# Kernel optimization log

Hardware: AMD Instinct MI355X
Metric: run time of the kernel (lower is better)

## Reference

```python
import jax, jax.numpy as jnp
import numpy as np

H = 768            # hidden_size
IMG_H = 1024       # image_hidden_size
NH = 12            # num_heads
NKV = 1            # num_kv_heads (MQA)
HD = H // NH       # head_dim = 64
FF = 4 * H         # intermediate_size = 3072
EPS = 1e-5


def layernorm(x, g, b):
    m = jnp.mean(x, axis=-1, keepdims=True)
    v = jnp.mean(jnp.square(x - m), axis=-1, keepdims=True)
    return (x - m) * jax.lax.rsqrt(v + EPS) * g + b


def setup_inputs() -> dict:
    key = jax.random.key(0)
    ks = jax.random.split(key, 12)
    B, NQ, NIMG = 8, 256, 4096
    s = 0.02
    return {
        "hidden_states": jax.random.normal(ks[0], (B, NQ, H), jnp.float32),
        "image_features": jax.random.normal(ks[1], (B, NIMG, IMG_H), jnp.float32),
        # norm_image_pre
        "ln_img_g": jnp.ones((IMG_H,), jnp.float32),
        "ln_img_b": jnp.zeros((IMG_H,), jnp.float32),
        # image_bottleneck (bias=False)
        "W_bottle": jax.random.normal(ks[2], (IMG_H, H), jnp.float32) * s,
        # norm_hidden
        "ln_h_g": jnp.ones((H,), jnp.float32),
        "ln_h_b": jnp.zeros((H,), jnp.float32),
        # to_q
        "Wq": jax.random.normal(ks[3], (H, H), jnp.float32) * s,
        "bq": jnp.zeros((H,), jnp.float32),
        # to_kv: out = num_kv_heads * head_dim * 2
        "Wkv": jax.random.normal(ks[4], (H, 2 * NKV * HD), jnp.float32) * s,
        "bkv": jnp.zeros((2 * NKV * HD,), jnp.float32),
        # to_out
        "Wo": jax.random.normal(ks[5], (H, H), jnp.float32) * s,
        "bo": jnp.zeros((H,), jnp.float32),
        # attn_out_norm
        "ln_ao_g": jnp.ones((H,), jnp.float32),
        "ln_ao_b": jnp.zeros((H,), jnp.float32),
        # gate
        "gate_param": jnp.zeros((), jnp.float32),
        # ffn_norm
        "ln_f_g": jnp.ones((H,), jnp.float32),
        "ln_f_b": jnp.zeros((H,), jnp.float32),
        # ffn
        "W1": jax.random.normal(ks[6], (H, FF), jnp.float32) * s,
        "b1": jnp.zeros((FF,), jnp.float32),
        "W2": jax.random.normal(ks[7], (FF, H), jnp.float32) * s,
        "b2": jnp.zeros((H,), jnp.float32),
    }


def reference(hidden_states, image_features, ln_img_g, ln_img_b, W_bottle,
              ln_h_g, ln_h_b, Wq, bq, Wkv, bkv, Wo, bo, ln_ao_g, ln_ao_b,
              gate_param, ln_f_g, ln_f_b, W1, b1, W2, b2):
    B, NQ, _ = hidden_states.shape
    # image pre-norm + bottleneck
    img = layernorm(image_features, ln_img_g, ln_img_b)
    img = img @ W_bottle                                   # [B, Nimg, H]
    # query path
    q_in = layernorm(hidden_states, ln_h_g, ln_h_b)
    q = (q_in @ Wq + bq).reshape(B, NQ, NH, HD).transpose(0, 2, 1, 3)  # b h i d
    # kv path (MQA: single shared KV head)
    kv = (img @ Wkv + bkv).reshape(B, -1, 2, NKV, HD)
    k = kv[:, :, 0, 0, :]                                  # [B, Nimg, HD]
    v = kv[:, :, 1, 0, :]
    scale = 1.0 / np.sqrt(HD)
    # broadcast KV across heads instead of explicit repeat
    scores = jnp.einsum('bhid,bjd->bhij', q * scale, k)    # [B, NH, NQ, Nimg]
    attn = jax.nn.softmax(scores, axis=-1)                 # dropout is identity (eval)
    out = jnp.einsum('bhij,bjd->bhid', attn, v)
    out = out.transpose(0, 2, 1, 3).reshape(B, NQ, H)
    out = out @ Wo + bo
    out = layernorm(out, ln_ao_g, ln_ao_b)
    gate = jax.nn.sigmoid(gate_param)
    h = hidden_states + gate * out
    ffn_in = layernorm(h, ln_f_g, ln_f_b)
    ffn_out = jax.nn.gelu(ffn_in @ W1 + b1, approximate=False) @ W2 + b2
    return h + ffn_out
```

## Files before the change

### kernel.cpp

```cpp
#include <hip/hip_runtime.h>
#include <cstdint>

typedef unsigned short u16;
typedef __bf16 bf16_t;
typedef bf16_t bf16x8 __attribute__((ext_vector_type(8)));
typedef float f32x4 __attribute__((ext_vector_type(4)));

__device__ __forceinline__ float b2f(u16 v) {
  union { uint32_t u; float f; } c; c.u = ((uint32_t)v) << 16; return c.f;
}
__device__ __forceinline__ u16 f2b(float f) {
  union { float f; uint32_t u; } c; c.f = f;
  uint32_t lsb = (c.u >> 16) & 1u;
  return (u16)((c.u + 0x7fffu + lsb) >> 16);
}
__device__ __forceinline__ uint4 pack8(f32x4 a, f32x4 b) {
  union { uint4 v; u16 s[8]; } r;
  r.s[0] = f2b(a[0]); r.s[1] = f2b(a[1]); r.s[2] = f2b(a[2]); r.s[3] = f2b(a[3]);
  r.s[4] = f2b(b[0]); r.s[5] = f2b(b[1]); r.s[6] = f2b(b[2]); r.s[7] = f2b(b[3]);
  return r.v;
}
__device__ __forceinline__ uint32_t cvt_pk_bf16(float lo, float hi) {
  uint32_t r;
  asm("v_cvt_pk_bf16_f32 %0, %1, %2" : "=v"(r) : "v"(lo), "v"(hi));
  return r;
}
__device__ __forceinline__ void phase_barrier() {
  asm volatile("s_waitcnt lgkmcnt(0)" ::: "memory");
  __builtin_amdgcn_s_barrier();
  asm volatile("" ::: "memory");
}
__device__ __forceinline__ void vm_drain() {
  asm volatile("s_waitcnt vmcnt(0)" ::: "memory");
}
template <int N>
__device__ __forceinline__ void vmwait() {
  asm volatile("s_waitcnt vmcnt(%0)" :: "n"(N) : "memory");
}
__device__ __forceinline__ void gload_lds16(const u16* g, u16* l) {
  __builtin_amdgcn_global_load_lds((const __attribute__((address_space(1))) void*)g,
                                   (__attribute__((address_space(3))) void*)l, 16, 0, 0);
}
__device__ __forceinline__ int xcd_swizzle(int lid, int nwg) {
  int q = nwg >> 3, r = nwg & 7, x = lid & 7, s = lid >> 3;
  return (x < r ? x * (q + 1) : r * (q + 1) + (x - r) * q) + s;
}

__global__ __launch_bounds__(256) void transpose_all(
    const float* __restrict__ Wq, const float* __restrict__ Wo, const float* __restrict__ W1,
    const float* __restrict__ W2, const float* __restrict__ Wkv,
    u16* __restrict__ WTq, u16* __restrict__ WTo, u16* __restrict__ WT1,
    u16* __restrict__ WT2, u16* __restrict__ WkvT) {
  __shared__ __align__(16) u16 tile[32][33];
  int bid = blockIdx.x;
  const float* in; u16* out; int R, C, gx, tb;
  if (bid < 576)       { in = Wq;  out = WTq;  R = 768;  C = 768;  gx = 24; tb = bid; }
  else if (bid < 1152) { in = Wo;  out = WTo;  R = 768;  C = 768;  gx = 24; tb = bid - 576; }
  else if (bid < 3456) { in = W1;  out = WT1;  R = 768;  C = 3072; gx = 96; tb = bid - 1152; }
  else if (bid < 5760) { in = W2;  out = WT2;  R = 3072; C = 768;  gx = 24; tb = bid - 3456; }
  else                 { in = Wkv; out = WkvT; R = 768;  C = 128;  gx = 4;  tb = bid - 5760; }
  int c0 = (tb % gx) * 32, r0 = (tb / gx) * 32;
  int tx = threadIdx.x & 31, ty = threadIdx.x >> 5;
#pragma unroll
  for (int i = 0; i < 4; ++i) {
    int r = r0 + ty + i * 8, c = c0 + tx;
    tile[ty + i * 8][tx] = f2b(in[(size_t)r * C + c]);
  }
  __syncthreads();
#pragma unroll
  for (int i = 0; i < 4; ++i) {
    int oc = c0 + ty + i * 8, orr = r0 + tx;
    out[(size_t)oc * R + orr] = tile[tx][ty + i * 8];
  }
}

__global__ __launch_bounds__(256) void prep_wg2(
    const u16* __restrict__ WTq, const float* __restrict__ gq, const float* __restrict__ bq_,
    u16* __restrict__ WqgT, float* __restrict__ uq, float* __restrict__ wq,
    const u16* __restrict__ WT1, const float* __restrict__ g1, const float* __restrict__ b1_,
    u16* __restrict__ W1gT, float* __restrict__ u1, float* __restrict__ w1) {
  int bid = blockIdx.x;
  const u16* WT; const float* g; const float* b; u16* WgT; float* u; float* w; int n0;
  if (bid < 192) { WT = WTq; g = gq; b = bq_; WgT = WqgT; u = uq; w = wq; n0 = bid * 4; }
  else { WT = WT1; g = g1; b = b1_; WgT = W1gT; u = u1; w = w1; n0 = (bid - 192) * 4; }
  int n = n0 + (threadIdx.x >> 6);
  int lane = threadIdx.x & 63;
  const u16* src = WT + (size_t)n * 768;
  u16* dst = WgT + (size_t)n * 768;
  float su = 0.f, sw = 0.f;
  for (int k = lane; k < 768; k += 64) {
    float wc = b2f(src[k]);
    float wg = g[k] * wc;
    dst[k] = f2b(wg);
    su += wg;
    sw += b[k] * wc;
  }
#pragma unroll
  for (int off = 32; off >= 1; off >>= 1) {
    su += __shfl_xor(su, off, 64);
    sw += __shfl_xor(sw, off, 64);
  }
  if (lane == 0) { u[n] = su; w[n] = sw; }
}

__global__ __launch_bounds__(256) void prep_wg(const u16* __restrict__ WT, const float* __restrict__ g,
                                               const float* __restrict__ b, u16* __restrict__ WgT,
                                               float* __restrict__ ucol, float* __restrict__ wcol,
                                               int K) {
  int n = blockIdx.x * 4 + (threadIdx.x >> 6);
  int lane = threadIdx.x & 63;
  const u16* src = WT + (size_t)n * K;
  u16* dst = WgT + (size_t)n * K;
  float su = 0.f, sw = 0.f;
  for (int k = lane; k < K; k += 64) {
    float wc = b2f(src[k]);
    float wg = g[k] * wc;
    dst[k] = f2b(wg);
    su += wg;
    sw += b[k] * wc;
  }
#pragma unroll
  for (int off = 32; off >= 1; off >>= 1) {
    su += __shfl_xor(su, off, 64);
    sw += __shfl_xor(sw, off, 64);
  }
  if (lane == 0) { ucol[n] = su; wcol[n] = sw; }
}

__global__ __launch_bounds__(256) void rowprep(
    const float* __restrict__ hs, u16* __restrict__ hs16,
    float* __restrict__ rstdq, float* __restrict__ mrstdq,
    const float* __restrict__ img, u16* __restrict__ img16,
    float* __restrict__ rstdi, float* __restrict__ mrstdi) {
  int bid = blockIdx.x, w = threadIdx.x >> 6, lane = threadIdx.x & 63;
  if (bid < 512) {
    int row = bid * 4 + w;
    const float* x = hs + (size_t)row * 768;
    float v[12];
#pragma unroll
    for (int it = 0; it < 3; ++it) {
      f32x4 d = *(const f32x4*)(x + (lane + it * 64) * 4);
      v[it * 4 + 0] = d[0]; v[it * 4 + 1] = d[1]; v[it * 4 + 2] = d[2]; v[it * 4 + 3] = d[3];
    }
    float s = 0.f, s2 = 0.f;
#pragma unroll
    for (int i = 0; i < 12; ++i) { s += v[i]; s2 += v[i] * v[i]; }
#pragma unroll
    for (int off = 32; off >= 1; off >>= 1) {
      s += __shfl_xor(s, off, 64);
      s2 += __shfl_xor(s2, off, 64);
    }
    float inv_n = 1.0f / 768.f;
    float mean = s * inv_n;
    float var = fmaxf(s2 * inv_n - mean * mean, 0.f);
    float rstd = rsqrtf(var + 1e-5f);
    if (lane == 0) { rstdq[row] = rstd; mrstdq[row] = mean * rstd; }
#pragma unroll
    for (int it = 0; it < 3; ++it) {
      int c = (lane + it * 64) * 4;
      uint2 po;
      po.x = (uint32_t)f2b(v[it * 4 + 0]) | ((uint32_t)f2b(v[it * 4 + 1]) << 16);
      po.y = (uint32_t)f2b(v[it * 4 + 2]) | ((uint32_t)f2b(v[it * 4 + 3]) << 16);
      *(uint2*)(hs16 + (size_t)row * 768 + c) = po;
    }
  } else {
    int row = (bid - 512) * 4 + w;
    const float* x = img + (size_t)row * 1024;
    float v[16];
#pragma unroll
    for (int it = 0; it < 4; ++it) {
      f32x4 d = *(const f32x4*)(x + (lane + it * 64) * 4);
      v[it * 4 + 0] = d[0]; v[it * 4 + 1] = d[1]; v[it * 4 + 2] = d[2]; v[it * 4 + 3] = d[3];
    }
    float s = 0.f, s2 = 0.f;
#pragma unroll
    for (int i = 0; i < 16; ++i) { s += v[i]; s2 += v[i] * v[i]; }
#pragma unroll
    for (int off = 32; off >= 1; off >>= 1) {
      s += __shfl_xor(s, off, 64);
      s2 += __shfl_xor(s2, off, 64);
    }
    float inv_n = 1.0f / 1024.f;
    float mean = s * inv_n;
    float var = fmaxf(s2 * inv_n - mean * mean, 0.f);
    float rstd = rsqrtf(var + 1e-5f);
    if (lane == 0) { rstdi[row] = rstd; mrstdi[row] = mean * rstd; }
#pragma unroll
    for (int it = 0; it < 4; ++it) {
      int c = (lane + it * 64) * 4;
      uint2 po;
      po.x = (uint32_t)f2b(v[it * 4 + 0]) | ((uint32_t)f2b(v[it * 4 + 1]) << 16);
      po.y = (uint32_t)f2b(v[it * 4 + 2]) | ((uint32_t)f2b(v[it * 4 + 3]) << 16);
      *(uint2*)(img16 + (size_t)row * 1024 + c) = po;
    }
  }
}

__global__ __launch_bounds__(256) void ln_res(const u16* __restrict__ ao, const float* __restrict__ g,
                                              const float* __restrict__ bta,
                                              const float* __restrict__ hs,
                                              const float* __restrict__ gatep,
                                              float* __restrict__ hf, u16* __restrict__ hb,
                                              float* __restrict__ rstdg, float* __restrict__ mrstdg) {
  int row = blockIdx.x * 4 + (threadIdx.x >> 6);
  int lane = threadIdx.x & 63;
  const u16* xb = ao + (size_t)row * 768;
  float v[12];
#pragma unroll
  for (int it = 0; it < 3; ++it) {
    int c = (lane + it * 64) * 4;
    uint2 d = *(const uint2*)(xb + c);
    v[it * 4 + 0] = b2f(d.x & 0xffff); v[it * 4 + 1] = b2f(d.x >> 16);
    v[it * 4 + 2] = b2f(d.y & 0xffff); v[it * 4 + 3] = b2f(d.y >> 16);
  }
  float s = 0.f, s2 = 0.f;
#pragma unroll
  for (int i = 0; i < 12; ++i) { s += v[i]; s2 += v[i] * v[i]; }
#pragma unroll
  for (int off = 32; off >= 1; off >>= 1) {
    s += __shfl_xor(s, off, 64);
    s2 += __shfl_xor(s2, off, 64);
  }
  float inv_n = 1.0f / 768.f;
  float mean = s * inv_n;
  float var = fmaxf(s2 * inv_n - mean * mean, 0.f);
  float rstd = rsqrtf(var + 1e-5f);
  float gate = 1.f / (1.f + __expf(-gatep[0]));
  float hsum = 0.f, hsum2 = 0.f;
  float o[12];
#pragma unroll
  for (int it = 0; it < 3; ++it) {
    int c = (lane + it * 64) * 4;
    const float* rr = hs + (size_t)row * 768 + c;
#pragma unroll
    for (int i = 0; i < 4; ++i) {
      float hv = rr[i] + gate * ((v[it * 4 + i] - mean) * rstd * g[c + i] + bta[c + i]);
      o[it * 4 + i] = hv;
      hsum += hv; hsum2 += hv * hv;
    }
    *(f32x4*)(hf + (size_t)row * 768 + c) = (f32x4){o[it * 4 + 0], o[it * 4 + 1], o[it * 4 + 2], o[it * 4 + 3]};
    uint2 po;
    po.x = (uint32_t)f2b(o[it * 4 + 0]) | ((uint32_t)f2b(o[it * 4 + 1]) << 16);
    po.y = (uint32_t)f2b(o[it * 4 + 2]) | ((uint32_t)f2b(o[it * 4 + 3]) << 16);
    *(uint2*)(hb + (size_t)row * 768 + c) = po;
  }
#pragma unroll
  for (int off = 32; off >= 1; off >>= 1) {
    hsum += __shfl_xor(hsum, off, 64);
    hsum2 += __shfl_xor(hsum2, off, 64);
  }
  float hm = hsum * inv_n;
  float hvar = fmaxf(hsum2 * inv_n - hm * hm, 0.f);
  float hrstd = rsqrtf(hvar + 1e-5f);
  if (lane == 0) { rstdg[row] = hrstd; mrstdg[row] = hm * hrstd; }
}

template <int BM, int SPLITK, int AMODE, int BMODE, int EPI, bool OUTF32, bool VTOUT>
__device__ __forceinline__ void gemm_body(const void* __restrict__ Av, const void* __restrict__ Bv,
                                          const float* __restrict__ bias,
                                          const float* __restrict__ rstdg,
                                          const float* __restrict__ mrstdg,
                                          const float* __restrict__ ucol,
                                          const float* __restrict__ wcol,
                                          void* __restrict__ Cv, u16* __restrict__ VTout,
                                          int M, int N, int K) {
  constexpr int MT = BM / 32;
  constexpr int AL = BM / 64;
  constexpr bool PURE = (AMODE == 0 && BMODE == 0);
  constexpr int NBUF = PURE ? 4 : 2;
  constexpr int LPT = AL + 2;
  __shared__ __align__(16) u16 aT[NBUF][BM * 32];
  __shared__ __align__(16) u16 bT[NBUF][128 * 32];

  int gx = gridDim.x, gy = gridDim.y;
  int nwg = gx * gy * (int)gridDim.z;
  int lid = ((int)blockIdx.z * gy + (int)blockIdx.y) * gx + (int)blockIdx.x;
  int wid = xcd_swizzle(lid, nwg);
  int bz = wid / (gx * gy);
  int rem = wid - bz * (gx * gy);
  int bx = rem / gy;
  int by = rem - bx * gy;

  int t = threadIdx.x, lane = t & 63, wave = t >> 6;
  int quad = lane >> 4, lcol = lane & 15;
  int wm = (wave >> 1) * (16 * MT), wn = (wave & 1) * 64;
  const u16* Ab = (const u16*)Av;
  const u16* Bb = (const u16*)Bv;
  const float* Bf = (const float*)Bv;
  const int kchunk = (SPLITK > 1) ? K / SPLITK : K;
  const int kstart = (SPLITK > 1) ? bz * kchunk : 0;
  int rr = t >> 1, rc = t & 1;
  f32x4 acc[MT][4];
#pragma unroll
  for (int i = 0; i < MT; ++i)
#pragma unroll
    for (int j = 0; j < 4; ++j) acc[i][j] = (f32x4){0.f, 0.f, 0.f, 0.f};

  f32x4 braw[4];

  auto dmaA = [&](int buf, int k0) {
#pragma unroll
    for (int s2 = 0; s2 < AL; ++s2) {
      int row = (wave * AL + s2) * 16 + (lane >> 2);
      int ch = (lane & 3) ^ (row & 3);
      gload_lds16(Ab + (size_t)(bx * BM + row) * K + kstart + k0 + ch * 8,
                  &aT[buf][(wave * AL + s2) * 512]);
    }
  };
  auto dmaB = [&](int buf, int k0) {
#pragma unroll
    for (int s2 = 0; s2 < 2; ++s2) {
      int row = (wave * 2 + s2) * 16 + (lane >> 2);
      int ch = (lane & 3) ^ (row & 3);
      gload_lds16(Bb + (size_t)(by * 128 + row) * K + kstart + k0 + ch * 8,
                  &bT[buf][(wave * 2 + s2) * 512]);
    }
  };
  auto regloadB = [&](int k0) {
    const f32x4* p = (const f32x4*)&Bf[(size_t)(by * 128 + rr) * K + kstart + k0 + rc * 16];
#pragma unroll
    for (int i = 0; i < 4; ++i) braw[i] = p[i];
  };
  auto regstoreB = [&](int buf) {
    uint4 c0 = pack8(braw[0], braw[1]), c1 = pack8(braw[2], braw[3]);
    *(uint4*)&bT[buf][rr * 32 + (((rc * 2 + 0) ^ (rr & 3)) << 3)] = c0;
    *(uint4*)&bT[buf][rr * 32 + (((rc * 2 + 1) ^ (rr & 3)) << 3)] = c1;
  };
  auto compute = [&](int buf) {
    bf16x8 af[MT], bfr[4];
#pragma unroll
    for (int mt = 0; mt < MT; ++mt) {
      int r = wm + mt * 16 + lcol;
      af[mt] = *(const bf16x8*)&aT[buf][r * 32 + (((quad ^ (r & 3))) << 3)];
    }
#pragma unroll
    for (int nt = 0; nt < 4; ++nt) {
      int r = wn + nt * 16 + lcol;
      bfr[nt] = *(const bf16x8*)&bT[buf][r * 32 + (((quad ^ (r & 3))) << 3)];
    }
#pragma unroll
    for (int mt = 0; mt < MT; ++mt)
#pragma unroll
      for (int nt = 0; nt < 4; ++nt)
        acc[mt][nt] = __builtin_amdgcn_mfma_f32_16x16x32_bf16(af[mt], bfr[nt], acc[mt][nt], 0, 0, 0);
  };

  const int nk = kchunk >> 5;
  if (PURE) {
    dmaA(0, 0); dmaB(0, 0);
    if (nk > 1) { dmaA(1, 1 << 5); dmaB(1, 1 << 5); }
    if (nk > 2) { dmaA(2, 2 << 5); dmaB(2, 2 << 5); }
    for (int kt = 0; kt < nk; ++kt) {
      int left = nk - 1 - kt;
      if (left >= 2) vmwait<2 * LPT>();
      else if (left == 1) vmwait<LPT>();
      else vmwait<0>();
      phase_barrier();
      if (kt + 3 < nk) { dmaA((kt + 3) & 3, (kt + 3) << 5); dmaB((kt + 3) & 3, (kt + 3) << 5); }
      compute(kt & 3);
    }
  } else {
    dmaA(0, 0);
    regloadB(0);
    regstoreB(0);
    vm_drain();
    phase_barrier();
    int cur = 0;
    for (int kt = 0; kt < nk; ++kt) {
      bool more = kt + 1 < nk;
      if (more) { dmaA(cur ^ 1, (kt + 1) << 5); regloadB((kt + 1) << 5); }
      compute(cur);
      if (more) regstoreB(cur ^ 1);
      vm_drain();
      phase_barrier();
      cur ^= 1;
    }
  }

  if (VTOUT) {
    __syncthreads();
    u16* vtile = &aT[0][0];
    u16* kb = (u16*)Cv;
#pragma unroll
    for (int mt = 0; mt < MT; ++mt) {
#pragma unroll
      for (int nt = 0; nt < 4; ++nt) {
#pragma unroll
        for (int r = 0; r < 4; ++r) {
          int lrow = wm + mt * 16 + quad * 4 + r;
          int row = bx * BM + lrow;
          int col = wn + nt * 16 + lcol;
          float v = rstdg[row] * acc[mt][nt][r] - mrstdg[row] * ucol[col] + wcol[col] + bias[col];
          u16 hv = f2b(v);
          if (wn == 0) kb[(size_t)row * 64 + col] = hv;
          else vtile[(col - 64) * 136 + lrow] = hv;
        }
      }
    }
    __syncthreads();
    int dd = t >> 2, js = (t & 3) * 32;
    int bg = bx >> 5, j0g = (bx & 31) * 128;
    u16* dst = VTout + ((size_t)bg * 64 + dd) * 4096 + j0g + js;
#pragma unroll
    for (int i = 0; i < 4; ++i)
      *(uint4*)(dst + i * 8) = *(const uint4*)&vtile[dd * 136 + js + i * 8];
    return;
  }

  u16* Cb = (u16*)Cv;
  float* Cf = (float*)Cv;
  if (SPLITK > 1) Cf += (size_t)bz * (size_t)M * (size_t)N;
#pragma unroll
  for (int mt = 0; mt < MT; ++mt) {
#pragma unroll
    for (int nt = 0; nt < 4; ++nt) {
#pragma unroll
      for (int r = 0; r < 4; ++r) {
        int lrow = wm + mt * 16 + quad * 4 + r;
        int row = bx * BM + lrow;
        int col = by * 128 + wn + nt * 16 + lcol;
        float v = acc[mt][nt][r];
        if (EPI == 1) v += bias[col];
        if (EPI == 3 || EPI == 5)
          v = rstdg[row] * v - mrstdg[row] * ucol[col] + wcol[col] + bias[col];
        if (EPI == 5) v = 0.5f * v * (1.f + erff(v * 0.70710678118f));
        size_t idx = (size_t)row * N + col;
        if (OUTF32) Cf[idx] = v; else Cb[idx] = f2b(v);
      }
    }
  }
}

#define GEMM_ARGS const void* Av, const void* Bv, const float* bias, const float* rstdg, \
                  const float* mrstdg, const float* ucol, const float* wcol, void* Cv,   \
                  u16* VTout, int M, int N, int K
__global__ __launch_bounds__(256) void gemm_wc(GEMM_ARGS) {
  gemm_body<128, 1, 0, 1, 0, false, false>(Av, Bv, bias, rstdg, mrstdg, ucol, wcol, Cv, VTout, M, N, K);
}
__global__ __launch_bounds__(256) void gemm_kv(GEMM_ARGS) {
  gemm_body<128, 1, 0, 0, 3, false, true>(Av, Bv, bias, rstdg, mrstdg, ucol, wcol, Cv, VTout, M, N, K);
}
__global__ __launch_bounds__(256) void gemm_q(GEMM_ARGS) {
  gemm_body<64, 1, 0, 0, 3, false, false>(Av, Bv, bias, rstdg, mrstdg, ucol, wcol, Cv, VTout, M, N, K);
}
__global__ __launch_bounds__(256) void gemm_o(GEMM_ARGS) {
  gemm_body<64, 1, 0, 0, 1, false, false>(Av, Bv, bias, rstdg, mrstdg, ucol, wcol, Cv, VTout, M, N, K);
}
__global__ __launch_bounds__(256) void gemm_w1(GEMM_ARGS) {
  gemm_body<128, 1, 0, 0, 5, false, false>(Av, Bv, bias, rstdg, mrstdg, ucol, wcol, Cv, VTout, M, N, K);
}
__global__ __launch_bounds__(256) void gemm_w2(GEMM_ARGS) {
  gemm_body<128, 2, 0, 0, 0, true, false>(Av, Bv, bias, rstdg, mrstdg, ucol, wcol, Cv, VTout, M, N, K);
}

__global__ __launch_bounds__(256) void w2_merge(const float* __restrict__ part,
                                                const float* __restrict__ hf,
                                                const float* __restrict__ b2,
                                                float* __restrict__ out) {
  int idx = blockIdx.x * 256 + threadIdx.x;
  f32x4 p0 = ((const f32x4*)part)[idx];
  f32x4 p1 = ((const f32x4*)part)[idx + 393216];
  f32x4 h = ((const f32x4*)hf)[idx];
  f32x4 bb = ((const f32x4*)b2)[idx % 192];
  f32x4 o;
#pragma unroll
  for (int i = 0; i < 4; ++i) o[i] = p0[i] + p1[i] + h[i] + bb[i];
  ((f32x4*)out)[idx] = o;
}

__global__ __launch_bounds__(256) void attn_kernel(const u16* __restrict__ qbuf,
                                                   const u16* __restrict__ kb,
                                                   const u16* __restrict__ VT,
                                                   float* __restrict__ Opart,
                                                   float* __restrict__ lpart) {
  __shared__ __align__(16) u16 k_lds[2][64 * 72];
  __shared__ __align__(16) u16 vt_lds[2][64 * 72];
  __shared__ __align__(16) u16 p_lds[4 * 16 * 72];
  int lid = ((int)blockIdx.z * 6 + (int)blockIdx.y) * 4 + (int)blockIdx.x;
  int wid = (lid & 7) * 96 + (lid >> 3);
  int bi = wid & 3;
  int hp = (wid >> 2) % 6;
  int z = wid / 24;
  int b = z >> 2, s = z & 3;
  int t = threadIdx.x;
  int wave = t >> 6, lane = t & 63, quad = lane >> 4, lcol = lane & 15;
  int i0 = bi * 64 + wave * 16;
  bf16x8 qf[2][2];
#pragma unroll
  for (int h2 = 0; h2 < 2; ++h2) {
    const u16* qrow = qbuf + ((size_t)(b * 256 + i0 + lcol) * 768 + (hp * 2 + h2) * 64 + quad * 8);
    qf[h2][0] = *(const bf16x8*)qrow;
    qf[h2][1] = *(const bf16x8*)(qrow + 32);
  }
  float l_r[2][4] = {{0.f, 0.f, 0.f, 0.f}, {0.f, 0.f, 0.f, 0.f}};
  f32x4 oacc[2][4];
#pragma unroll
  for (int h2 = 0; h2 < 2; ++h2)
#pragma unroll
    for (int nt = 0; nt < 4; ++nt) oacc[h2][nt] = (f32x4){0.f, 0.f, 0.f, 0.f};
  int sr = t >> 2, sc = (t & 3) * 16;
  const u16* kbase = kb + (size_t)b * 4096 * 64;
  const u16* vtbase = VT + (size_t)b * 64 * 4096;
  u16* pw = &p_lds[wave * 16 * 72];

  uint4 kr0, kr1, vr0, vr1;
  auto stage_load = [&](int jt) {
    int j0 = s * 1024 + jt * 64;
    const u16* krow = kbase + (size_t)(j0 + sr) * 64 + sc;
    kr0 = *(const uint4*)(krow);
    kr1 = *(const uint4*)(krow + 8);
    const u16* vrow = vtbase + (size_t)sr * 4096 + j0 + sc;
    vr0 = *(const uint4*)(vrow);
    vr1 = *(const uint4*)(vrow + 8);
  };
  auto stage_store = [&](int buf) {
    *(uint4*)&k_lds[buf][sr * 72 + sc] = kr0;
    *(uint4*)&k_lds[buf][sr * 72 + sc + 8] = kr1;
    *(uint4*)&vt_lds[buf][sr * 72 + sc] = vr0;
    *(uint4*)&vt_lds[buf][sr * 72 + sc + 8] = vr1;
  };

  stage_load(0);
  stage_store(0);
  phase_barrier();
  int cur = 0;
  for (int jt = 0; jt < 16; ++jt) {
    bool more = jt + 1 < 16;
    if (more) stage_load(jt + 1);

#pragma unroll
    for (int h2 = 0; h2 < 2; ++h2) {
      f32x4 sc4[4];
#pragma unroll
      for (int nt = 0; nt < 4; ++nt) sc4[nt] = (f32x4){0.f, 0.f, 0.f, 0.f};
      __builtin_amdgcn_s_setprio(1);
#pragma unroll
      for (int nt = 0; nt < 4; ++nt) {
        bf16x8 kb0 = *(const bf16x8*)&k_lds[cur][(nt * 16 + lcol) * 72 + quad * 8];
        bf16x8 kb1 = *(const bf16x8*)&k_lds[cur][(nt * 16 + lcol) * 72 + 32 + quad * 8];
        sc4[nt] = __builtin_amdgcn_mfma_f32_16x16x32_bf16(qf[h2][0], kb0, sc4[nt], 0, 0, 0);
        sc4[nt] = __builtin_amdgcn_mfma_f32_16x16x32_bf16(qf[h2][1], kb1, sc4[nt], 0, 0, 0);
      }
      __builtin_amdgcn_s_setprio(0);
#pragma unroll
      for (int r = 0; r < 4; ++r) {
        float rsum = 0.f;
#pragma unroll
        for (int nt = 0; nt < 4; ++nt) {
          float p = __expf(sc4[nt][r] * 0.125f);
          sc4[nt][r] = p;
          rsum += p;
        }
        rsum += __shfl_xor(rsum, 1, 64);
        rsum += __shfl_xor(rsum, 2, 64);
        rsum += __shfl_xor(rsum, 4, 64);
        rsum += __shfl_xor(rsum, 8, 64);
        l_r[h2][r] += rsum;
        uint32_t pk01 = cvt_pk_bf16(sc4[0][r], sc4[1][r]);
        uint32_t pk23 = cvt_pk_bf16(sc4[2][r], sc4[3][r]);
        int prow = (quad * 4 + r) * 72 + lcol;
        pw[prow] = (u16)(pk01 & 0xffff);
        pw[prow + 16] = (u16)(pk01 >> 16);
        pw[prow + 32] = (u16)(pk23 & 0xffff);
        pw[prow + 48] = (u16)(pk23 >> 16);
      }
      __builtin_amdgcn_s_setprio(1);
#pragma unroll
      for (int ks = 0; ks < 2; ++ks) {
        bf16x8 pa = *(const bf16x8*)&pw[lcol * 72 + ks * 32 + quad * 8];
#pragma unroll
        for (int nt = 0; nt < 4; ++nt) {
          bf16x8 vb = *(const bf16x8*)&vt_lds[cur][(nt * 16 + lcol) * 72 + ks * 32 + quad * 8];
          oacc[h2][nt] = __builtin_amdgcn_mfma_f32_16x16x32_bf16(pa, vb, oacc[h2][nt], 0, 0, 0);
        }
      }
      __builtin_amdgcn_s_setprio(0);
    }
    if (more) stage_store(cur ^ 1);
    phase_barrier();
    cur ^= 1;
  }
#pragma unroll
  for (int h2 = 0; h2 < 2; ++h2) {
    size_t base = ((size_t)z * 12 + hp * 2 + h2) * 256;
#pragma unroll
    for (int r = 0; r < 4; ++r) {
      int row = bi * 64 + wave * 16 + quad * 4 + r;
#pragma unroll
      for (int nt = 0; nt < 4; ++nt)
        Opart[(base + row) * 64 + nt * 16 + lcol] = oacc[h2][nt][r];
      if (lcol == 0) lpart[base + row] = l_r[h2][r];
    }
  }
}

__global__ __launch_bounds__(256) void attn_merge(const float* __restrict__ Opart,
                                                  const float* __restrict__ lpart,
                                                  u16* __restrict__ attn_o) {
  int row = blockIdx.x;
  int col = blockIdx.y * 256 + threadIdx.x;
  int b = row >> 8, i = row & 255, h = col >> 6, d = col & 63;
  float o = 0.f, l = 0.f;
#pragma unroll
  for (int s = 0; s < 4; ++s) {
    size_t ii = (((size_t)(b * 4 + s) * 12 + h) * 256 + i);
    o += Opart[ii * 64 + d];
    l += lpart[ii];
  }
  attn_o[(size_t)row * 768 + col] = f2b(o / l);
}

extern "C" void kernel_launch(void* const* d_in, const int* in_sizes, int n_in, void* d_out,
                              int out_size, void* d_ws, size_t ws_size, hipStream_t stream) {
  (void)in_sizes; (void)n_in; (void)out_size; (void)ws_size;
  const float* hs = (const float*)d_in[0];
  const float* imgf = (const float*)d_in[1];
  const float* ln_img_g = (const float*)d_in[2];
  const float* ln_img_b = (const float*)d_in[3];
  const float* W_bottle = (const float*)d_in[4];
  const float* ln_h_g = (const float*)d_in[5];
  const float* ln_h_b = (const float*)d_in[6];
  const float* Wq = (const float*)d_in[7];
  const float* bq = (const float*)d_in[8];
  const float* Wkv = (const float*)d_in[9];
  const float* bkv = (const float*)d_in[10];
  const float* Wo = (const float*)d_in[11];
  const float* bo = (const float*)d_in[12];
  const float* ln_ao_g = (const float*)d_in[13];
  const float* ln_ao_b = (const float*)d_in[14];
  const float* gatep = (const float*)d_in[15];
  const float* ln_f_g = (const float*)d_in[16];
  const float* ln_f_b = (const float*)d_in[17];
  const float* W1 = (const float*)d_in[18];
  const float* b1 = (const float*)d_in[19];
  const float* W2 = (const float*)d_in[20];
  const float* b2 = (const float*)d_in[21];

  char* sc = (char*)d_ws;
  auto alloc = [&](size_t bytes) {
    char* p = sc;
    sc += (bytes + 63) & ~(size_t)63;
    return p;
  };
  u16* WTq = (u16*)alloc(768 * 768 * 2);
  u16* WTo = (u16*)alloc(768 * 768 * 2);
  u16* WT1 = (u16*)alloc(3072 * 768 * 2);
  u16* WT2 = (u16*)alloc(768 * 3072 * 2);
  u16* WkvT = (u16*)alloc(128 * 768 * 2);
  u16* WcT = (u16*)alloc(128 * 1024 * 2);
  u16* WgT = (u16*)alloc(128 * 1024 * 2);
  u16* WqgT = (u16*)alloc(768 * 768 * 2);
  u16* W1gT = (u16*)alloc(3072 * 768 * 2);
  float* ucol = (float*)alloc(128 * 4);
  float* wcol = (float*)alloc(128 * 4);
  float* uq = (float*)alloc(768 * 4);
  float* wq = (float*)alloc(768 * 4);
  float* u1 = (float*)alloc(3072 * 4);
  float* w1c = (float*)alloc(3072 * 4);
  float* rstdq = (float*)alloc(2048 * 4);
  float* mrstdq = (float*)alloc(2048 * 4);
  float* rstdh = (float*)alloc(2048 * 4);
  float* mrstdh = (float*)alloc(2048 * 4);
  float* rstdi = (float*)alloc(32768 * 4);
  float* mrstdi = (float*)alloc(32768 * 4);
  u16* hs16 = (u16*)alloc(2048 * 768 * 2);
  u16* img16 = (u16*)alloc((size_t)32768 * 1024 * 2);
  u16* kb = (u16*)alloc((size_t)32768 * 64 * 2);
  u16* VT = (u16*)alloc((size_t)8 * 64 * 4096 * 2);
  u16* qb = (u16*)alloc(2048 * 768 * 2);
  u16* attn_o = (u16*)alloc(2048 * 768 * 2);
  u16* ao = (u16*)alloc(2048 * 768 * 2);
  u16* hbuf = (u16*)alloc(2048 * 768 * 2);
  float* hf32 = (float*)alloc(2048 * 768 * 4);
  u16* actb = (u16*)alloc((size_t)2048 * 3072 * 2);
  float* Opart = (float*)alloc((size_t)32 * 12 * 256 * 64 * 4);
  float* lpart = (float*)alloc((size_t)32 * 12 * 256 * 4);

  transpose_all<<<5856, 256, 0, stream>>>(Wq, Wo, W1, W2, Wkv, WTq, WTo, WT1, WT2, WkvT);
  prep_wg2<<<960, 256, 0, stream>>>(WTq, ln_h_g, ln_h_b, WqgT, uq, wq,
                                    WT1, ln_f_g, ln_f_b, W1gT, u1, w1c);
  gemm_wc<<<dim3(1, 8), 256, 0, stream>>>(WkvT, W_bottle, nullptr, nullptr, nullptr, nullptr,
                                          nullptr, WcT, nullptr, 128, 1024, 768);
  prep_wg<<<32, 256, 0, stream>>>(WcT, ln_img_g, ln_img_b, WgT, ucol, wcol, 1024);
  rowprep<<<8704, 256, 0, stream>>>(hs, hs16, rstdq, mrstdq, imgf, img16, rstdi, mrstdi);
  gemm_kv<<<dim3(256, 1), 256, 0, stream>>>(img16, WgT, bkv, rstdi, mrstdi, ucol, wcol,
                                            kb, VT, 32768, 128, 1024);
  gemm_q<<<dim3(32, 6), 256, 0, stream>>>(hs16, WqgT, bq, rstdq, mrstdq, uq, wq,
                                          qb, nullptr, 2048, 768, 768);
  attn_kernel<<<dim3(4, 6, 32), 256, 0, stream>>>(qb, kb, VT, Opart, lpart);
  attn_merge<<<dim3(2048, 3), 256, 0, stream>>>(Opart, lpart, attn_o);
  gemm_o<<<dim3(32, 6), 256, 0, stream>>>(attn_o, WTo, bo, nullptr, nullptr, nullptr, nullptr,
                                          ao, nullptr, 2048, 768, 768);
  ln_res<<<512, 256, 0, stream>>>(ao, ln_ao_g, ln_ao_b, hs, gatep, hf32, hbuf, rstdh, mrstdh);
  gemm_w1<<<dim3(16, 24), 256, 0, stream>>>(hbuf, W1gT, b1, rstdh, mrstdh, u1, w1c,
                                            actb, nullptr, 2048, 3072, 768);
  gemm_w2<<<dim3(16, 6, 2), 256, 0, stream>>>(actb, WT2, nullptr, nullptr, nullptr, nullptr, nullptr,
                                              Opart, nullptr, 2048, 768, 3072);
  w2_merge<<<1536, 256, 0, stream>>>(Opart, hf32, b2, (float*)d_out);
}
```

Baseline: 532.9 us.

## Fuse prep kernels, merge KV and Q GEMMs, fold attention merge into out-projection

The weight transpose and row-normalisation prep kernels become one launch, and the KV and Q projection GEMMs share a single grid through virtual block indexing. The attention split-K merge (summing partial outputs and dividing by the row sum) now happens inside the out-projection GEMM's A-tile loader, which removes the separate merge kernel and its bf16 intermediate buffer. The attention kernel now handles one head per block instead of two, doubling its grid in y. The aim is fewer launches and less global round-tripping, at the cost of a heavier register-path A load in gemm_o and some imbalance between the heterogeneous blocks in the fused launches.

```diff
diff --git a/kernel.cpp b/kernel.cpp
--- a/kernel.cpp
+++ b/kernel.cpp
@@ -46,45 +46,112 @@
   return (x < r ? x * (q + 1) : r * (q + 1) + (x - r) * q) + s;
 }
 
-__global__ __launch_bounds__(256) void transpose_all(
+__global__ __launch_bounds__(256) void prep_main(
     const float* __restrict__ Wq, const float* __restrict__ Wo, const float* __restrict__ W1,
     const float* __restrict__ W2, const float* __restrict__ Wkv,
     u16* __restrict__ WTq, u16* __restrict__ WTo, u16* __restrict__ WT1,
-    u16* __restrict__ WT2, u16* __restrict__ WkvT) {
+    u16* __restrict__ WT2, u16* __restrict__ WkvT,
+    const float* __restrict__ hs, u16* __restrict__ hs16,
+    float* __restrict__ rstdq, float* __restrict__ mrstdq,
+    const float* __restrict__ img, u16* __restrict__ img16,
+    float* __restrict__ rstdi, float* __restrict__ mrstdi) {
   __shared__ __align__(16) u16 tile[32][33];
   int bid = blockIdx.x;
-  const float* in; u16* out; int R, C, gx, tb;
-  if (bid < 576)       { in = Wq;  out = WTq;  R = 768;  C = 768;  gx = 24; tb = bid; }
-  else if (bid < 1152) { in = Wo;  out = WTo;  R = 768;  C = 768;  gx = 24; tb = bid - 576; }
-  else if (bid < 3456) { in = W1;  out = WT1;  R = 768;  C = 3072; gx = 96; tb = bid - 1152; }
-  else if (bid < 5760) { in = W2;  out = WT2;  R = 3072; C = 768;  gx = 24; tb = bid - 3456; }
-  else                 { in = Wkv; out = WkvT; R = 768;  C = 128;  gx = 4;  tb = bid - 5760; }
-  int c0 = (tb % gx) * 32, r0 = (tb / gx) * 32;
-  int tx = threadIdx.x & 31, ty = threadIdx.x >> 5;
-#pragma unroll
-  for (int i = 0; i < 4; ++i) {
-    int r = r0 + ty + i * 8, c = c0 + tx;
-    tile[ty + i * 8][tx] = f2b(in[(size_t)r * C + c]);
-  }
-  __syncthreads();
-#pragma unroll
-  for (int i = 0; i < 4; ++i) {
-    int oc = c0 + ty + i * 8, orr = r0 + tx;
-    out[(size_t)oc * R + orr] = tile[tx][ty + i * 8];
-  }
-}
-
-__global__ __launch_bounds__(256) void prep_wg2(
+  int lane = threadIdx.x & 63, w = threadIdx.x >> 6;
+  if (bid < 5856) {
+    const float* in; u16* out; int R, C, gx, tb;
+    if (bid < 576)       { in = Wq;  out = WTq;  R = 768;  C = 768;  gx = 24; tb = bid; }
+    else if (bid < 1152) { in = Wo;  out = WTo;  R = 768;  C = 768;  gx = 24; tb = bid - 576; }
+    else if (bid < 3456) { in = W1;  out = WT1;  R = 768;  C = 3072; gx = 96; tb = bid - 1152; }
+    else if (bid < 5760) { in = W2;  out = WT2;  R = 3072; C = 768;  gx = 24; tb = bid - 3456; }
+    else                 { in = Wkv; out = WkvT; R = 768;  C = 128;  gx = 4;  tb = bid - 5760; }
+    int c0 = (tb % gx) * 32, r0 = (tb / gx) * 32;
+    int tx = threadIdx.x & 31, ty = threadIdx.x >> 5;
+#pragma unroll
+    for (int i = 0; i < 4; ++i) {
+      int r = r0 + ty + i * 8, c = c0 + tx;
+      tile[ty + i * 8][tx] = f2b(in[(size_t)r * C + c]);
+    }
+    __syncthreads();
+#pragma unroll
+    for (int i = 0; i < 4; ++i) {
+      int oc = c0 + ty + i * 8, orr = r0 + tx;
+      out[(size_t)oc * R + orr] = tile[tx][ty + i * 8];
+    }
+  } else if (bid < 6368) {
+    int row = (bid - 5856) * 4 + w;
+    const float* x = hs + (size_t)row * 768;
+    float v[12];
+#pragma unroll
+    for (int it = 0; it < 3; ++it) {
+      f32x4 d = *(const f32x4*)(x + (lane + it * 64) * 4);
+      v[it * 4 + 0] = d[0]; v[it * 4 + 1] = d[1]; v[it * 4 + 2] = d[2]; v[it * 4 + 3] = d[3];
+    }
+    float s = 0.f, s2 = 0.f;
+#pragma unroll
+    for (int i = 0; i < 12; ++i) { s += v[i]; s2 += v[i] * v[i]; }
+#pragma unroll
+    for (int off = 32; off >= 1; off >>= 1) {
+      s += __shfl_xor(s, off, 64);
+      s2 += __shfl_xor(s2, off, 64);
+    }
+    float inv_n = 1.0f / 768.f;
+    float mean = s * inv_n;
+    float var = fmaxf(s2 * inv_n - mean * mean, 0.f);
+    float rstd = rsqrtf(var + 1e-5f);
+    if (lane == 0) { rstdq[row] = rstd; mrstdq[row] = mean * rstd; }
+#pragma unroll
+    for (int it = 0; it < 3; ++it) {
+      int c = (lane + it * 64) * 4;
+      uint2 po;
+      po.x = (uint32_t)f2b(v[it * 4 + 0]) | ((uint32_t)f2b(v[it * 4 + 1]) << 16);
+      po.y = (uint32_t)f2b(v[it * 4 + 2]) | ((uint32_t)f2b(v[it * 4 + 3]) << 16);
+      *(uint2*)(hs16 + (size_t)row * 768 + c) = po;
+    }
+  } else {
+    int row = (bid - 6368) * 4 + w;
+    const float* x = img + (size_t)row * 1024;
+    float v[16];
+#pragma unroll
+    for (int it = 0; it < 4; ++it) {
+      f32x4 d = *(const f32x4*)(x + (lane + it * 64) * 4);
+      v[it * 4 + 0] = d[0]; v[it * 4 + 1] = d[1]; v[it * 4 + 2] = d[2]; v[it * 4 + 3] = d[3];
+    }
+    float s = 0.f, s2 = 0.f;
+#pragma unroll
+    for (int i = 0; i < 16; ++i) { s += v[i]; s2 += v[i] * v[i]; }
+#pragma unroll
+    for (int off = 32; off >= 1; off >>= 1) {
+      s += __shfl_xor(s, off, 64);
+      s2 += __shfl_xor(s2, off, 64);
+    }
+    float inv_n = 1.0f / 1024.f;
+    float mean = s * inv_n;
+    float var = fmaxf(s2 * inv_n - mean * mean, 0.f);
+    float rstd = rsqrtf(var + 1e-5f);
+    if (lane == 0) { rstdi[row] = rstd; mrstdi[row] = mean * rstd; }
+#pragma unroll
+    for (int it = 0; it < 4; ++it) {
+      int c = (lane + it * 64) * 4;
+      uint2 po;
+      po.x = (uint32_t)f2b(v[it * 4 + 0]) | ((uint32_t)f2b(v[it * 4 + 1]) << 16);
+      po.y = (uint32_t)f2b(v[it * 4 + 2]) | ((uint32_t)f2b(v[it * 4 + 3]) << 16);
+      *(uint2*)(img16 + (size_t)row * 1024 + c) = po;
+    }
+  }
+}
+
+__global__ __launch_bounds__(256) void prep_fold(
     const u16* __restrict__ WTq, const float* __restrict__ gq, const float* __restrict__ bq_,
-    u16* __restrict__ WqgT, float* __restrict__ uq, float* __restrict__ wq,
+    u16* __restrict__ WqgT, float* __restrict__ uq, float* __restrict__ wqv,
     const u16* __restrict__ WT1, const float* __restrict__ g1, const float* __restrict__ b1_,
-    u16* __restrict__ W1gT, float* __restrict__ u1, float* __restrict__ w1) {
-  int bid = blockIdx.x;
-  const u16* WT; const float* g; const float* b; u16* WgT; float* u; float* w; int n0;
-  if (bid < 192) { WT = WTq; g = gq; b = bq_; WgT = WqgT; u = uq; w = wq; n0 = bid * 4; }
-  else { WT = WT1; g = g1; b = b1_; WgT = W1gT; u = u1; w = w1; n0 = (bid - 192) * 4; }
-  int n = n0 + (threadIdx.x >> 6);
-  int lane = threadIdx.x & 63;
+    u16* __restrict__ W1gT, float* __restrict__ u1, float* __restrict__ w1v) {
+  int pid = blockIdx.x;
+  int lane = threadIdx.x & 63, w = threadIdx.x >> 6;
+  const u16* WT; const float* g; const float* b; u16* WgT; float* u; float* wv; int n0;
+  if (pid < 192) { WT = WTq; g = gq; b = bq_; WgT = WqgT; u = uq; wv = wqv; n0 = pid * 4; }
+  else { WT = WT1; g = g1; b = b1_; WgT = W1gT; u = u1; wv = w1v; n0 = (pid - 192) * 4; }
+  int n = n0 + w;
   const u16* src = WT + (size_t)n * 768;
   u16* dst = WgT + (size_t)n * 768;
   float su = 0.f, sw = 0.f;
@@ -100,7 +167,7 @@
     su += __shfl_xor(su, off, 64);
     sw += __shfl_xor(sw, off, 64);
   }
-  if (lane == 0) { u[n] = su; w[n] = sw; }
+  if (lane == 0) { u[n] = su; wv[n] = sw; }
 }
 
 __global__ __launch_bounds__(256) void prep_wg(const u16* __restrict__ WT, const float* __restrict__ g,
@@ -127,75 +194,6 @@
   if (lane == 0) { ucol[n] = su; wcol[n] = sw; }
 }
 
-__global__ __launch_bounds__(256) void rowprep(
-    const float* __restrict__ hs, u16* __restrict__ hs16,
-    float* __restrict__ rstdq, float* __restrict__ mrstdq,
-    const float* __restrict__ img, u16* __restrict__ img16,
-    float* __restrict__ rstdi, float* __restrict__ mrstdi) {
-  int bid = blockIdx.x, w = threadIdx.x >> 6, lane = threadIdx.x & 63;
-  if (bid < 512) {
-    int row = bid * 4 + w;
-    const float* x = hs + (size_t)row * 768;
-    float v[12];
-#pragma unroll
-    for (int it = 0; it < 3; ++it) {
-      f32x4 d = *(const f32x4*)(x + (lane + it * 64) * 4);
-      v[it * 4 + 0] = d[0]; v[it * 4 + 1] = d[1]; v[it * 4 + 2] = d[2]; v[it * 4 + 3] = d[3];
-    }
-    float s = 0.f, s2 = 0.f;
-#pragma unroll
-    for (int i = 0; i < 12; ++i) { s += v[i]; s2 += v[i] * v[i]; }
-#pragma unroll
-    for (int off = 32; off >= 1; off >>= 1) {
-      s += __shfl_xor(s, off, 64);
-      s2 += __shfl_xor(s2, off, 64);
-    }
-    float inv_n = 1.0f / 768.f;
-    float mean = s * inv_n;
-    float var = fmaxf(s2 * inv_n - mean * mean, 0.f);
-    float rstd = rsqrtf(var + 1e-5f);
-    if (lane == 0) { rstdq[row] = rstd; mrstdq[row] = mean * rstd; }
-#pragma unroll
-    for (int it = 0; it < 3; ++it) {
-      int c = (lane + it * 64) * 4;
-      uint2 po;
-      po.x = (uint32_t)f2b(v[it * 4 + 0]) | ((uint32_t)f2b(v[it * 4 + 1]) << 16);
-      po.y = (uint32_t)f2b(v[it * 4 + 2]) | ((uint32_t)f2b(v[it * 4 + 3]) << 16);
-      *(uint2*)(hs16 + (size_t)row * 768 + c) = po;
-    }
-  } else {
-    int row = (bid - 512) * 4 + w;
-    const float* x = img + (size_t)row * 1024;
-    float v[16];
-#pragma unroll
-    for (int it = 0; it < 4; ++it) {
-      f32x4 d = *(const f32x4*)(x + (lane + it * 64) * 4);
-      v[it * 4 + 0] = d[0]; v[it * 4 + 1] = d[1]; v[it * 4 + 2] = d[2]; v[it * 4 + 3] = d[3];
-    }
-    float s = 0.f, s2 = 0.f;
-#pragma unroll
-    for (int i = 0; i < 16; ++i) { s += v[i]; s2 += v[i] * v[i]; }
-#pragma unroll
-    for (int off = 32; off >= 1; off >>= 1) {
-      s += __shfl_xor(s, off, 64);
-      s2 += __shfl_xor(s2, off, 64);
-    }
-    float inv_n = 1.0f / 1024.f;
-    float mean = s * inv_n;
-    float var = fmaxf(s2 * inv_n - mean * mean, 0.f);
-    float rstd = rsqrtf(var + 1e-5f);
-    if (lane == 0) { rstdi[row] = rstd; mrstdi[row] = mean * rstd; }
-#pragma unroll
-    for (int it = 0; it < 4; ++it) {
-      int c = (lane + it * 64) * 4;
-      uint2 po;
-      po.x = (uint32_t)f2b(v[it * 4 + 0]) | ((uint32_t)f2b(v[it * 4 + 1]) << 16);
-      po.y = (uint32_t)f2b(v[it * 4 + 2]) | ((uint32_t)f2b(v[it * 4 + 3]) << 16);
-      *(uint2*)(img16 + (size_t)row * 1024 + c) = po;
-    }
-  }
-}
-
 __global__ __launch_bounds__(256) void ln_res(const u16* __restrict__ ao, const float* __restrict__ g,
                                               const float* __restrict__ bta,
                                               const float* __restrict__ hs,
@@ -256,35 +254,36 @@
 }
 
 template <int BM, int SPLITK, int AMODE, int BMODE, int EPI, bool OUTF32, bool VTOUT>
-__device__ __forceinline__ void gemm_body(const void* __restrict__ Av, const void* __restrict__ Bv,
+__device__ __forceinline__ void gemm_body(u16* __restrict__ aTb, u16* __restrict__ bTb,
+                                          const void* __restrict__ Av, const void* __restrict__ Bv,
                                           const float* __restrict__ bias,
                                           const float* __restrict__ rstdg,
                                           const float* __restrict__ mrstdg,
                                           const float* __restrict__ ucol,
                                           const float* __restrict__ wcol,
+                                          const float* __restrict__ auxl,
                                           void* __restrict__ Cv, u16* __restrict__ VTout,
-                                          int M, int N, int K) {
+                                          int M, int N, int K,
+                                          int vgx, int vgy, int vgz, int vlid) {
   constexpr int MT = BM / 32;
   constexpr int AL = BM / 64;
   constexpr bool PURE = (AMODE == 0 && BMODE == 0);
-  constexpr int NBUF = PURE ? 4 : 2;
   constexpr int LPT = AL + 2;
-  __shared__ __align__(16) u16 aT[NBUF][BM * 32];
-  __shared__ __align__(16) u16 bT[NBUF][128 * 32];
-
-  int gx = gridDim.x, gy = gridDim.y;
-  int nwg = gx * gy * (int)gridDim.z;
-  int lid = ((int)blockIdx.z * gy + (int)blockIdx.y) * gx + (int)blockIdx.x;
-  int wid = xcd_swizzle(lid, nwg);
-  int bz = wid / (gx * gy);
-  int rem = wid - bz * (gx * gy);
-  int bx = rem / gy;
-  int by = rem - bx * gy;
+  constexpr int ASZ = BM * 32;
+  constexpr int BSZ = 128 * 32;
+
+  int nwg = vgx * vgy * vgz;
+  int wid = xcd_swizzle(vlid, nwg);
+  int bz = wid / (vgx * vgy);
+  int rem = wid - bz * (vgx * vgy);
+  int bx = rem / vgy;
+  int by = rem - bx * vgy;
 
   int t = threadIdx.x, lane = t & 63, wave = t >> 6;
   int quad = lane >> 4, lcol = lane & 15;
   int wm = (wave >> 1) * (16 * MT), wn = (wave & 1) * 64;
   const u16* Ab = (const u16*)Av;
+  const float* Af = (const float*)Av;
   const u16* Bb = (const u16*)Bv;
   const float* Bf = (const float*)Bv;
   const int kchunk = (SPLITK > 1) ? K / SPLITK : K;
@@ -297,6 +296,7 @@
     for (int j = 0; j < 4; ++j) acc[i][j] = (f32x4){0.f, 0.f, 0.f, 0.f};
 
   f32x4 braw[4];
+  f32x4 am0, am1;
 
   auto dmaA = [&](int buf, int k0) {
 #pragma unroll
@@ -304,7 +304,7 @@
       int row = (wave * AL + s2) * 16 + (lane >> 2);
       int ch = (lane & 3) ^ (row & 3);
       gload_lds16(Ab + (size_t)(bx * BM + row) * K + kstart + k0 + ch * 8,
-                  &aT[buf][(wave * AL + s2) * 512]);
+                  aTb + buf * ASZ + (wave * AL + s2) * 512);
     }
   };
   auto dmaB = [&](int buf, int k0) {
@@ -313,8 +313,34 @@
       int row = (wave * 2 + s2) * 16 + (lane >> 2);
       int ch = (lane & 3) ^ (row & 3);
       gload_lds16(Bb + (size_t)(by * 128 + row) * K + kstart + k0 + ch * 8,
-                  &bT[buf][(wave * 2 + s2) * 512]);
-    }
+                  bTb + buf * BSZ + (wave * 2 + s2) * 512);
+    }
+  };
+  auto loadAmerge = [&](int k0) {
+    int c0 = kstart + k0 + (t & 3) * 8;
+    int hh = c0 >> 6, dd = c0 & 63;
+    int row = bx * 64 + (t >> 2);
+    int bb = row >> 8, ii = row & 255;
+    am0 = (f32x4){0.f, 0.f, 0.f, 0.f};
+    am1 = (f32x4){0.f, 0.f, 0.f, 0.f};
+    float lsum = 0.f;
+#pragma unroll
+    for (int s = 0; s < 4; ++s) {
+      size_t base = ((size_t)((bb * 4 + s) * 12 + hh)) * 256 + ii;
+      const f32x4* p = (const f32x4*)(Af + base * 64 + dd);
+      f32x4 p0 = p[0], p1 = p[1];
+#pragma unroll
+      for (int j = 0; j < 4; ++j) { am0[j] += p0[j]; am1[j] += p1[j]; }
+      lsum += auxl[base];
+    }
+    float rl = 1.f / lsum;
+#pragma unroll
+    for (int j = 0; j < 4; ++j) { am0[j] *= rl; am1[j] *= rl; }
+  };
+  auto storeAmerge = [&](int buf) {
+    uint4 c = pack8(am0, am1);
+    int ar = t >> 2, ch = t & 3;
+    *(uint4*)(aTb + buf * ASZ + ar * 32 + ((ch ^ (ar & 3)) << 3)) = c;
   };
   auto regloadB = [&](int k0) {
     const f32x4* p = (const f32x4*)&Bf[(size_t)(by * 128 + rr) * K + kstart + k0 + rc * 16];
@@ -323,20 +349,20 @@
   };
   auto regstoreB = [&](int buf) {
     uint4 c0 = pack8(braw[0], braw[1]), c1 = pack8(braw[2], braw[3]);
-    *(uint4*)&bT[buf][rr * 32 + (((rc * 2 + 0) ^ (rr & 3)) << 3)] = c0;
-    *(uint4*)&bT[buf][rr * 32 + (((rc * 2 + 1) ^ (rr & 3)) << 3)] = c1;
+    *(uint4*)(bTb + buf * BSZ + rr * 32 + (((rc * 2 + 0) ^ (rr & 3)) << 3)) = c0;
+    *(uint4*)(bTb + buf * BSZ + rr * 32 + (((rc * 2 + 1) ^ (rr & 3)) << 3)) = c1;
   };
   auto compute = [&](int buf) {
     bf16x8 af[MT], bfr[4];
 #pragma unroll
     for (int mt = 0; mt < MT; ++mt) {
       int r = wm + mt * 16 + lcol;
-      af[mt] = *(const bf16x8*)&aT[buf][r * 32 + (((quad ^ (r & 3))) << 3)];
+      af[mt] = *(const bf16x8*)(aTb + buf * ASZ + r * 32 + (((quad ^ (r & 3))) << 3));
     }
 #pragma unroll
     for (int nt = 0; nt < 4; ++nt) {
       int r = wn + nt * 16 + lcol;
-      bfr[nt] = *(const bf16x8*)&bT[buf][r * 32 + (((quad ^ (r & 3))) << 3)];
+      bfr[nt] = *(const bf16x8*)(bTb + buf * BSZ + r * 32 + (((quad ^ (r & 3))) << 3));
     }
 #pragma unroll
     for (int mt = 0; mt < MT; ++mt)
@@ -360,17 +386,24 @@
       compute(kt & 3);
     }
   } else {
-    dmaA(0, 0);
-    regloadB(0);
-    regstoreB(0);
+    if (AMODE == 2) loadAmerge(0); else dmaA(0, 0);
+    if (BMODE == 1) regloadB(0); else dmaB(0, 0);
+    if (AMODE == 2) storeAmerge(0);
+    if (BMODE == 1) regstoreB(0);
     vm_drain();
     phase_barrier();
     int cur = 0;
     for (int kt = 0; kt < nk; ++kt) {
       bool more = kt + 1 < nk;
-      if (more) { dmaA(cur ^ 1, (kt + 1) << 5); regloadB((kt + 1) << 5); }
+      if (more) {
+        if (AMODE == 2) loadAmerge((kt + 1) << 5); else dmaA(cur ^ 1, (kt + 1) << 5);
+        if (BMODE == 1) regloadB((kt + 1) << 5); else dmaB(cur ^ 1, (kt + 1) << 5);
+      }
       compute(cur);
-      if (more) regstoreB(cur ^ 1);
+      if (more) {
+        if (AMODE == 2) storeAmerge(cur ^ 1);
+        if (BMODE == 1) regstoreB(cur ^ 1);
+      }
       vm_drain();
       phase_barrier();
       cur ^= 1;
@@ -379,7 +412,7 @@
 
   if (VTOUT) {
     __syncthreads();
-    u16* vtile = &aT[0][0];
+    u16* vtile = aTb;
     u16* kb = (u16*)Cv;
 #pragma unroll
     for (int mt = 0; mt < MT; ++mt) {
@@ -431,26 +464,53 @@
   }
 }
 
-#define GEMM_ARGS const void* Av, const void* Bv, const float* bias, const float* rstdg, \
-                  const float* mrstdg, const float* ucol, const float* wcol, void* Cv,   \
-                  u16* VTout, int M, int N, int K
-__global__ __launch_bounds__(256) void gemm_wc(GEMM_ARGS) {
-  gemm_body<128, 1, 0, 1, 0, false, false>(Av, Bv, bias, rstdg, mrstdg, ucol, wcol, Cv, VTout, M, N, K);
-}
-__global__ __launch_bounds__(256) void gemm_kv(GEMM_ARGS) {
-  gemm_body<128, 1, 0, 0, 3, false, true>(Av, Bv, bias, rstdg, mrstdg, ucol, wcol, Cv, VTout, M, N, K);
-}
-__global__ __launch_bounds__(256) void gemm_q(GEMM_ARGS) {
-  gemm_body<64, 1, 0, 0, 3, false, false>(Av, Bv, bias, rstdg, mrstdg, ucol, wcol, Cv, VTout, M, N, K);
-}
-__global__ __launch_bounds__(256) void gemm_o(GEMM_ARGS) {
-  gemm_body<64, 1, 0, 0, 1, false, false>(Av, Bv, bias, rstdg, mrstdg, ucol, wcol, Cv, VTout, M, N, K);
-}
-__global__ __launch_bounds__(256) void gemm_w1(GEMM_ARGS) {
-  gemm_body<128, 1, 0, 0, 5, false, false>(Av, Bv, bias, rstdg, mrstdg, ucol, wcol, Cv, VTout, M, N, K);
-}
-__global__ __launch_bounds__(256) void gemm_w2(GEMM_ARGS) {
-  gemm_body<128, 2, 0, 0, 0, true, false>(Av, Bv, bias, rstdg, mrstdg, ucol, wcol, Cv, VTout, M, N, K);
+__global__ __launch_bounds__(256) void gemm_wc(const void* Av, const void* Bv, void* Cv) {
+  __shared__ __align__(16) u16 lds[16384];
+  int vlid = ((int)blockIdx.y) * 1 + (int)blockIdx.x;
+  gemm_body<128, 1, 0, 1, 0, false, false>(lds, lds + 8192, Av, Bv, nullptr, nullptr, nullptr,
+                                           nullptr, nullptr, nullptr, Cv, nullptr,
+                                           128, 1024, 768, 1, 8, 1, vlid);
+}
+__global__ __launch_bounds__(256) void gemm_kvq(
+    const void* Akv, const void* Bkv, const float* biaskv, const float* rstdi,
+    const float* mrstdi, const float* ui, const float* wi, void* Ckv, u16* VTout,
+    const void* Aq, const void* Bq, const float* biasq, const float* rstdq,
+    const float* mrstdq, const float* uq, const float* wqv, void* Cq) {
+  __shared__ __align__(16) u16 lds[32768];
+  int bid = blockIdx.x;
+  if (bid < 256) {
+    gemm_body<128, 1, 0, 0, 3, false, true>(lds, lds + 16384, Akv, Bkv, biaskv, rstdi, mrstdi,
+                                            ui, wi, nullptr, Ckv, VTout,
+                                            32768, 128, 1024, 256, 1, 1, bid);
+  } else {
+    gemm_body<64, 1, 0, 0, 3, false, false>(lds, lds + 8192, Aq, Bq, biasq, rstdq, mrstdq,
+                                            uq, wqv, nullptr, Cq, nullptr,
+                                            2048, 768, 768, 32, 6, 1, bid - 256);
+  }
+}
+__global__ __launch_bounds__(256) void gemm_o(const void* Av, const void* Bv, const float* bias,
+                                              const float* lpart, void* Cv) {
+  __shared__ __align__(16) u16 lds[12288];
+  int vlid = ((int)blockIdx.y) * 32 + (int)blockIdx.x;
+  gemm_body<64, 1, 2, 0, 1, false, false>(lds, lds + 4096, Av, Bv, bias, nullptr, nullptr,
+                                          nullptr, nullptr, lpart, Cv, nullptr,
+                                          2048, 768, 768, 32, 6, 1, vlid);
+}
+__global__ __launch_bounds__(256) void gemm_w1(const void* Av, const void* Bv, const float* bias,
+                                               const float* rstdg, const float* mrstdg,
+                                               const float* ucol, const float* wcol, void* Cv) {
+  __shared__ __align__(16) u16 lds[32768];
+  int vlid = ((int)blockIdx.y) * 16 + (int)blockIdx.x;
+  gemm_body<128, 1, 0, 0, 5, false, false>(lds, lds + 16384, Av, Bv, bias, rstdg, mrstdg,
+                                           ucol, wcol, nullptr, Cv, nullptr,
+                                           2048, 3072, 768, 16, 24, 1, vlid);
+}
+__global__ __launch_bounds__(256) void gemm_w2(const void* Av, const void* Bv, void* Cv) {
+  __shared__ __align__(16) u16 lds[32768];
+  int vlid = (((int)blockIdx.z) * 6 + (int)blockIdx.y) * 16 + (int)blockIdx.x;
+  gemm_body<128, 2, 0, 0, 0, true, false>(lds, lds + 16384, Av, Bv, nullptr, nullptr, nullptr,
+                                          nullptr, nullptr, nullptr, Cv, nullptr,
+                                          2048, 768, 3072, 16, 6, 2, vlid);
 }
 
 __global__ __launch_bounds__(256) void w2_merge(const float* __restrict__ part,
@@ -476,28 +536,22 @@
   __shared__ __align__(16) u16 k_lds[2][64 * 72];
   __shared__ __align__(16) u16 vt_lds[2][64 * 72];
   __shared__ __align__(16) u16 p_lds[4 * 16 * 72];
-  int lid = ((int)blockIdx.z * 6 + (int)blockIdx.y) * 4 + (int)blockIdx.x;
-  int wid = (lid & 7) * 96 + (lid >> 3);
+  int lid = ((int)blockIdx.z * 12 + (int)blockIdx.y) * 4 + (int)blockIdx.x;
+  int wid = (lid & 7) * 192 + (lid >> 3);
   int bi = wid & 3;
-  int hp = (wid >> 2) % 6;
-  int z = wid / 24;
+  int h = (wid >> 2) % 12;
+  int z = wid / 48;
   int b = z >> 2, s = z & 3;
   int t = threadIdx.x;
   int wave = t >> 6, lane = t & 63, quad = lane >> 4, lcol = lane & 15;
   int i0 = bi * 64 + wave * 16;
-  bf16x8 qf[2][2];
-#pragma unroll
-  for (int h2 = 0; h2 < 2; ++h2) {
-    const u16* qrow = qbuf + ((size_t)(b * 256 + i0 + lcol) * 768 + (hp * 2 + h2) * 64 + quad * 8);
-    qf[h2][0] = *(const bf16x8*)qrow;
-    qf[h2][1] = *(const bf16x8*)(qrow + 32);
-  }
-  float l_r[2][4] = {{0.f, 0.f, 0.f, 0.f}, {0.f, 0.f, 0.f, 0.f}};
-  f32x4 oacc[2][4];
-#pragma unroll
-  for (int h2 = 0; h2 < 2; ++h2)
-#pragma unroll
-    for (int nt = 0; nt < 4; ++nt) oacc[h2][nt] = (f32x4){0.f, 0.f, 0.f, 0.f};
+  const u16* qrow = qbuf + ((size_t)(b * 256 + i0 + lcol) * 768 + h * 64 + quad * 8);
+  bf16x8 qf0 = *(const bf16x8*)qrow;
+  bf16x8 qf1 = *(const bf16x8*)(qrow + 32);
+  float l_r[4] = {0.f, 0.f, 0.f, 0.f};
+  f32x4 oacc[4];
+#pragma unroll
+  for (int nt = 0; nt < 4; ++nt) oacc[nt] = (f32x4){0.f, 0.f, 0.f, 0.f};
   int sr = t >> 2, sc = (t & 3) * 16;
   const u16* kbase = kb + (size_t)b * 4096 * 64;
   const u16* vtbase = VT + (size_t)b * 64 * 4096;
@@ -528,86 +582,64 @@
     bool more = jt + 1 < 16;
     if (more) stage_load(jt + 1);
 
-#pragma unroll
-    for (int h2 = 0; h2 < 2; ++h2) {
-      f32x4 sc4[4];
-#pragma unroll
-      for (int nt = 0; nt < 4; ++nt) sc4[nt] = (f32x4){0.f, 0.f, 0.f, 0.f};
-      __builtin_amdgcn_s_setprio(1);
+    f32x4 sc4[4];
+#pragma unroll
+    for (int nt = 0; nt < 4; ++nt) sc4[nt] = (f32x4){0.f, 0.f, 0.f, 0.f};
+    __builtin_amdgcn_s_setprio(1);
+#pragma unroll
+    for (int nt = 0; nt < 4; ++nt) {
+      bf16x8 kb0 = *(const bf16x8*)&k_lds[cur][(nt * 16 + lcol) * 72 + quad * 8];
+      bf16x8 kb1 = *(const bf16x8*)&k_lds[cur][(nt * 16 + lcol) * 72 + 32 + quad * 8];
+      sc4[nt] = __builtin_amdgcn_mfma_f32_16x16x32_bf16(qf0, kb0, sc4[nt], 0, 0, 0);
+      sc4[nt] = __builtin_amdgcn_mfma_f32_16x16x32_bf16(qf1, kb1, sc4[nt], 0, 0, 0);
+    }
+    __builtin_amdgcn_s_setprio(0);
+#pragma unroll
+    for (int r = 0; r < 4; ++r) {
+      float rsum = 0.f;
 #pragma unroll
       for (int nt = 0; nt < 4; ++nt) {
-        bf16x8 kb0 = *(const bf16x8*)&k_lds[cur][(nt * 16 + lcol) * 72 + quad * 8];
-        bf16x8 kb1 = *(const bf16x8*)&k_lds[cur][(nt * 16 + lcol) * 72 + 32 + quad * 8];
-        sc4[nt] = __builtin_amdgcn_mfma_f32_16x16x32_bf16(qf[h2][0], kb0, sc4[nt], 0, 0, 0);
-        sc4[nt] = __builtin_amdgcn_mfma_f32_16x16x32_bf16(qf[h2][1], kb1, sc4[nt], 0, 0, 0);
+        float p = __expf(sc4[nt][r] * 0.125f);
+        sc4[nt][r] = p;
+        rsum += p;
       }
-      __builtin_amdgcn_s_setprio(0);
-#pragma unroll
-      for (int r = 0; r < 4; ++r) {
-        float rsum = 0.f;
-#pragma unroll
-        for (int nt = 0; nt < 4; ++nt) {
-          float p = __expf(sc4[nt][r] * 0.125f);
-          sc4[nt][r] = p;
-          rsum += p;
-        }
-        rsum += __shfl_xor(rsum, 1, 64);
-        rsum += __shfl_xor(rsum, 2, 64);
-        rsum += __shfl_xor(rsum, 4, 64);
-        rsum += __shfl_xor(rsum, 8, 64);
-        l_r[h2][r] += rsum;
-        uint32_t pk01 = cvt_pk_bf16(sc4[0][r], sc4[1][r]);
-        uint32_t pk23 = cvt_pk_bf16(sc4[2][r], sc4[3][r]);
-        int prow = (quad * 4 + r) * 72 + lcol;
-        pw[prow] = (u16)(pk01 & 0xffff);
-        pw[prow + 16] = (u16)(pk01 >> 16);
-        pw[prow + 32] = (u16)(pk23 & 0xffff);
-        pw[prow + 48] = (u16)(pk23 >> 16);
+      rsum += __shfl_xor(rsum, 1, 64);
+      rsum += __shfl_xor(rsum, 2, 64);
+      rsum += __shfl_xor(rsum, 4, 64);
+      rsum += __shfl_xor(rsum, 8, 64);
+      l_r[r] += rsum;
+      uint32_t pk01 = cvt_pk_bf16(sc4[0][r], sc4[1][r]);
+      uint32_t pk23 = cvt_pk_bf16(sc4[2][r], sc4[3][r]);
+      int prow = (quad * 4 + r) * 72 + lcol;
+      pw[prow] = (u16)(pk01 & 0xffff);
+      pw[prow + 16] = (u16)(pk01 >> 16);
+      pw[prow + 32] = (u16)(pk23 & 0xffff);
+      pw[prow + 48] = (u16)(pk23 >> 16);
+    }
+    __builtin_amdgcn_s_setprio(1);
+#pragma unroll
+    for (int ks = 0; ks < 2; ++ks) {
+      bf16x8 pa = *(const bf16x8*)&pw[lcol * 72 + ks * 32 + quad * 8];
+#pragma unroll
+      for (int nt = 0; nt < 4; ++nt) {
+        bf16x8 vb = *(const bf16x8*)&vt_lds[cur][(nt * 16 + lcol) * 72 + ks * 32 + quad * 8];
+        oacc[nt] = __builtin_amdgcn_mfma_f32_16x16x32_bf16(pa, vb, oacc[nt], 0, 0, 0);
       }
-      __builtin_amdgcn_s_setprio(1);
-#pragma unroll
-      for (int ks = 0; ks < 2; ++ks) {
-        bf16x8 pa = *(const bf16x8*)&pw[lcol * 72 + ks * 32 + quad * 8];
-#pragma unroll
-        for (int nt = 0; nt < 4; ++nt) {
-          bf16x8 vb = *(const bf16x8*)&vt_lds[cur][(nt * 16 + lcol) * 72 + ks * 32 + quad * 8];
-          oacc[h2][nt] = __builtin_amdgcn_mfma_f32_16x16x32_bf16(pa, vb, oacc[h2][nt], 0, 0, 0);
-        }
-      }
-      __builtin_amdgcn_s_setprio(0);
-    }
+    }
+    __builtin_amdgcn_s_setprio(0);
     if (more) stage_store(cur ^ 1);
     phase_barrier();
     cur ^= 1;
   }
-#pragma unroll
-  for (int h2 = 0; h2 < 2; ++h2) {
-    size_t base = ((size_t)z * 12 + hp * 2 + h2) * 256;
-#pragma unroll
-    for (int r = 0; r < 4; ++r) {
-      int row = bi * 64 + wave * 16 + quad * 4 + r;
-#pragma unroll
-      for (int nt = 0; nt < 4; ++nt)
-        Opart[(base + row) * 64 + nt * 16 + lcol] = oacc[h2][nt][r];
-      if (lcol == 0) lpart[base + row] = l_r[h2][r];
-    }
-  }
-}
-
-__global__ __launch_bounds__(256) void attn_merge(const float* __restrict__ Opart,
-                                                  const float* __restrict__ lpart,
-                                                  u16* __restrict__ attn_o) {
-  int row = blockIdx.x;
-  int col = blockIdx.y * 256 + threadIdx.x;
-  int b = row >> 8, i = row & 255, h = col >> 6, d = col & 63;
-  float o = 0.f, l = 0.f;
-#pragma unroll
-  for (int s = 0; s < 4; ++s) {
-    size_t ii = (((size_t)(b * 4 + s) * 12 + h) * 256 + i);
-    o += Opart[ii * 64 + d];
-    l += lpart[ii];
-  }
-  attn_o[(size_t)row * 768 + col] = f2b(o / l);
+  size_t base = ((size_t)z * 12 + h) * 256;
+#pragma unroll
+  for (int r = 0; r < 4; ++r) {
+    int row = bi * 64 + wave * 16 + quad * 4 + r;
+#pragma unroll
+    for (int nt = 0; nt < 4; ++nt)
+      Opart[(base + row) * 64 + nt * 16 + lcol] = oacc[nt][r];
+    if (lcol == 0) lpart[base + row] = l_r[r];
+  }
 }
 
 extern "C" void kernel_launch(void* const* d_in, const int* in_sizes, int n_in, void* d_out,
@@ -668,7 +700,6 @@
   u16* kb = (u16*)alloc((size_t)32768 * 64 * 2);
   u16* VT = (u16*)alloc((size_t)8 * 64 * 4096 * 2);
   u16* qb = (u16*)alloc(2048 * 768 * 2);
-  u16* attn_o = (u16*)alloc(2048 * 768 * 2);
   u16* ao = (u16*)alloc(2048 * 768 * 2);
   u16* hbuf = (u16*)alloc(2048 * 768 * 2);
   float* hf32 = (float*)alloc(2048 * 768 * 4);
@@ -676,25 +707,19 @@
   float* Opart = (float*)alloc((size_t)32 * 12 * 256 * 64 * 4);
   float* lpart = (float*)alloc((size_t)32 * 12 * 256 * 4);
 
-  transpose_all<<<5856, 256, 0, stream>>>(Wq, Wo, W1, W2, Wkv, WTq, WTo, WT1, WT2, WkvT);
-  prep_wg2<<<960, 256, 0, stream>>>(WTq, ln_h_g, ln_h_b, WqgT, uq, wq,
-                                    WT1, ln_f_g, ln_f_b, W1gT, u1, w1c);
-  gemm_wc<<<dim3(1, 8), 256, 0, stream>>>(WkvT, W_bottle, nullptr, nullptr, nullptr, nullptr,
-                                          nullptr, WcT, nullptr, 128, 1024, 768);
+  prep_main<<<14560, 256, 0, stream>>>(Wq, Wo, W1, W2, Wkv, WTq, WTo, WT1, WT2, WkvT,
+                                       hs, hs16, rstdq, mrstdq,
+                                       imgf, img16, rstdi, mrstdi);
+  prep_fold<<<960, 256, 0, stream>>>(WTq, ln_h_g, ln_h_b, WqgT, uq, wq,
+                                     WT1, ln_f_g, ln_f_b, W1gT, u1, w1c);
+  gemm_wc<<<dim3(1, 8), 256, 0, stream>>>(WkvT, W_bottle, WcT);
   prep_wg<<<32, 256, 0, stream>>>(WcT, ln_img_g, ln_img_b, WgT, ucol, wcol, 1024);
-  rowprep<<<8704, 256, 0, stream>>>(hs, hs16, rstdq, mrstdq, imgf, img16, rstdi, mrstdi);
-  gemm_kv<<<dim3(256, 1), 256, 0, stream>>>(img16, WgT, bkv, rstdi, mrstdi, ucol, wcol,
-                                            kb, VT, 32768, 128, 1024);
-  gemm_q<<<dim3(32, 6), 256, 0, stream>>>(hs16, WqgT, bq, rstdq, mrstdq, uq, wq,
-                                          qb, nullptr, 2048, 768, 768);
-  attn_kernel<<<dim3(4, 6, 32), 256, 0, stream>>>(qb, kb, VT, Opart, lpart);
-  attn_merge<<<dim3(2048, 3), 256, 0, stream>>>(Opart, lpart, attn_o);
-  gemm_o<<<dim3(32, 6), 256, 0, stream>>>(attn_o, WTo, bo, nullptr, nullptr, nullptr, nullptr,
-                                          ao, nullptr, 2048, 768, 768);
+  gemm_kvq<<<448, 256, 0, stream>>>(img16, WgT, bkv, rstdi, mrstdi, ucol, wcol, kb, VT,
+                                    hs16, WqgT, bq, rstdq, mrstdq, uq, wq, qb);
+  attn_kernel<<<dim3(4, 12, 32), 256, 0, stream>>>(qb, kb, VT, Opart, lpart);
+  gemm_o<<<dim3(32, 6), 256, 0, stream>>>(Opart, WTo, bo, lpart, ao);
   ln_res<<<512, 256, 0, stream>>>(ao, ln_ao_g, ln_ao_b, hs, gatep, hf32, hbuf, rstdh, mrstdh);
-  gemm_w1<<<dim3(16, 24), 256, 0, stream>>>(hbuf, W1gT, b1, rstdh, mrstdh, u1, w1c,
-                                            actb, nullptr, 2048, 3072, 768);
-  gemm_w2<<<dim3(16, 6, 2), 256, 0, stream>>>(actb, WT2, nullptr, nullptr, nullptr, nullptr, nullptr,
-                                              Opart, nullptr, 2048, 768, 3072);
+  gemm_w1<<<dim3(16, 24), 256, 0, stream>>>(hbuf, W1gT, b1, rstdh, mrstdh, u1, w1c, actb);
+  gemm_w2<<<dim3(16, 6, 2), 256, 0, stream>>>(actb, WT2, Opart);
   w2_merge<<<1536, 256, 0, stream>>>(Opart, hf32, b2, (float*)d_out);
 }
```

New measurement: 495.3 us. -7.1%, faster.
